# Kernel tuning notes

Hardware: AMD Instinct MI355X
Metric: run time of the kernel (lower is better)

## Reference

```python
import jax, jax.numpy as jnp
import numpy as np

D_MODEL = 1024
NUM_HEADS = 16
HEAD_DIM = D_MODEL // NUM_HEADS


def setup_inputs() -> dict:
    key = jax.random.key(0)
    ks = jax.random.split(key, 9)
    s = 0.02
    return {
        "x": jax.random.normal(ks[0], (4, 2048, D_MODEL), dtype=jnp.float32),
        "Wq": jax.random.normal(ks[1], (D_MODEL, D_MODEL), dtype=jnp.float32) * s,
        "bq": jnp.zeros((D_MODEL,), dtype=jnp.float32),
        "Wk": jax.random.normal(ks[2], (D_MODEL, D_MODEL), dtype=jnp.float32) * s,
        "bk": jnp.zeros((D_MODEL,), dtype=jnp.float32),
        "Wv": jax.random.normal(ks[3], (D_MODEL, D_MODEL), dtype=jnp.float32) * s,
        "bv": jnp.zeros((D_MODEL,), dtype=jnp.float32),
        "Wo": jax.random.normal(ks[4], (D_MODEL, D_MODEL), dtype=jnp.float32) * s,
        "bo": jnp.zeros((D_MODEL,), dtype=jnp.float32),
    }


def reference(x, Wq, bq, Wk, bk, Wv, bv, Wo, bo):
    B, S, D = x.shape
    H, Hd = NUM_HEADS, HEAD_DIM

    def split_heads(t):  # [B,S,D] -> [B,H,S,Hd]
        return t.reshape(B, S, H, Hd).transpose(0, 2, 1, 3)

    q = split_heads(x @ Wq + bq)
    k = split_heads(x @ Wk + bk)
    v = split_heads(x @ Wv + bv)

    scale = 1.0 / jnp.sqrt(jnp.float32(Hd))
    scores = jnp.einsum("bhqd,bhkd->bhqk", q, k) * scale  # [B,H,S,S]
    attn = jax.nn.softmax(scores, axis=-1)
    # dropout(p=0.1) is identity in eval mode
    ctx = jnp.einsum("bhqk,bhkd->bhqd", attn, v)
    ctx = ctx.transpose(0, 2, 1, 3).reshape(B, S, D)
    return ctx @ Wo + bo
```

## Files before the change

### kernel.cpp

```cpp
#include <hip/hip_runtime.h>
#include <hip/hip_bf16.h>

typedef __bf16 bf16;
typedef bf16 bf16x8 __attribute__((ext_vector_type(8)));
typedef bf16 bf16x4v __attribute__((ext_vector_type(4)));
typedef bf16 bf16x2v __attribute__((ext_vector_type(2)));
typedef float f32x4 __attribute__((ext_vector_type(4)));
typedef float f32x16 __attribute__((ext_vector_type(16)));
typedef unsigned int uint;
typedef uint uint4v __attribute__((ext_vector_type(4)));

#define D_MODEL 1024
#define SEQ     2048
#define BATCH   4
#define NHEAD   16
#define HDIM    64
#define MTOK    8192
#define RSZ     ((size_t)MTOK * D_MODEL)
#define QSCALE  0.18033688011112042f

#define GLD16(src, dst)                                                        \
  __builtin_amdgcn_global_load_lds(                                            \
      (const __attribute__((address_space(1))) void*)(src),                    \
      (__attribute__((address_space(3))) void*)(dst), 16, 0, 0)

#define WAITVM(N) asm volatile("s_waitcnt vmcnt(" #N ")" ::: "memory")
#define BAR() __builtin_amdgcn_s_barrier()

#define PSWAP(a, b) asm("v_permlane32_swap_b32 %0, %1" : "+v"(a), "+v"(b))

__device__ __forceinline__ uint pk2(float lo, float hi) {
  bf16x2v h;
  h[0] = (bf16)lo;
  h[1] = (bf16)hi;
  return __builtin_bit_cast(uint, h);
}

__global__ __launch_bounds__(256) void cvt_x_kernel(const float* __restrict__ x,
                                                    bf16* __restrict__ xb) {
  int i = blockIdx.x * 256 + threadIdx.x;
  f32x4 v = ((const f32x4*)x)[i];
  bf16x4v o;
#pragma unroll
  for (int c = 0; c < 4; ++c) o[c] = (bf16)v[c];
  ((bf16x4v*)xb)[i] = o;
}

__global__ __launch_bounds__(256) void wtrans_kernel(
    const float* __restrict__ Wq, const float* __restrict__ Wk,
    const float* __restrict__ Wv, const float* __restrict__ Wo,
    bf16* __restrict__ wt, bf16* __restrict__ wot) {
  __shared__ float t[32][33];
  int z = blockIdx.z;
  const float* W = (z == 0) ? Wq : (z == 1) ? Wk : (z == 2) ? Wv : Wo;
  bf16* dst = (z < 3) ? (wt + (size_t)z * D_MODEL * D_MODEL) : wot;
  int tx = threadIdx.x, ty = threadIdx.y;
  int bx = blockIdx.x * 32, by = blockIdx.y * 32;
#pragma unroll
  for (int j = 0; j < 4; ++j)
    t[ty + j * 8][tx] = W[(size_t)(by + ty + j * 8) * D_MODEL + bx + tx];
  __syncthreads();
#pragma unroll
  for (int j = 0; j < 4; ++j)
    dst[(size_t)(bx + ty + j * 8) * D_MODEL + by + tx] = (bf16)t[tx][ty + j * 8];
}

__global__ __launch_bounds__(256) void vtrans_kernel(const bf16* __restrict__ V,
                                                     bf16* __restrict__ Vt) {
  __shared__ bf16 Ls[128][72];
  const int st = blockIdx.x, bh = blockIdx.y;
  const bf16* src = V + ((size_t)bh * SEQ + st * 128) * HDIM;
  bf16* dst = Vt + (size_t)bh * HDIM * SEQ + st * 128;
  const int t = threadIdx.x;
  const int r = t >> 3, d0 = (t & 7) * 8;
#pragma unroll
  for (int j = 0; j < 4; ++j)
    *(bf16x8*)&Ls[r + j * 32][d0] = *(const bf16x8*)(src + (size_t)(r + j * 32) * HDIM + d0);
  __syncthreads();
  const int d = t & 63, sc = (t >> 6) * 32;
#pragma unroll
  for (int c = 0; c < 4; ++c) {
    bf16x8 v;
#pragma unroll
    for (int i = 0; i < 8; ++i) v[i] = Ls[sc + c * 8 + i][d];
    *(bf16x8*)(dst + (size_t)d * SEQ + sc + c * 8) = v;
  }
}

template <int MODE>
__global__ __launch_bounds__(256) void gemm_bt(
    const bf16* __restrict__ A, const bf16* __restrict__ Bt,
    const float* __restrict__ bias0, const float* __restrict__ bias1,
    const float* __restrict__ bias2, void* __restrict__ outp) {
  __shared__ bf16 As[128 * 32];
  __shared__ bf16 Bs[128 * 32];
  const int tid = threadIdx.x;
  const int wave = tid >> 6, lane = tid & 63;
  const int rowBase = blockIdx.y * 128;
  const int colBase = blockIdx.x * 128;
  const int wR = (wave >> 1) * 64;
  const int wC = (wave & 1) * 64;

  const int r0 = tid >> 2, c0 = tid & 3;
  const int cp0 = c0 ^ ((r0 >> 1) & 3);
  const int r1 = 64 + r0;
  const int cp1 = c0 ^ ((r1 >> 1) & 3);
  const bf16* srcA0 = A + (size_t)(rowBase + r0) * 1024 + cp0 * 8;
  const bf16* srcA1 = A + (size_t)(rowBase + r1) * 1024 + cp1 * 8;
  const bf16* srcB0 = Bt + (size_t)(colBase + r0) * 1024 + cp0 * 8;
  const bf16* srcB1 = Bt + (size_t)(colBase + r1) * 1024 + cp1 * 8;
  char* AsB = (char*)As;
  char* BsB = (char*)Bs;
  char* ldsA0 = AsB + wave * 1024;
  char* ldsA1 = AsB + 4096 + wave * 1024;
  char* ldsB0 = BsB + wave * 1024;
  char* ldsB1 = BsB + 4096 + wave * 1024;

  int aoff[4], boff[4];
#pragma unroll
  for (int i = 0; i < 4; ++i) {
    int ra = wR + i * 16 + (lane & 15);
    aoff[i] = ra * 64 + (((lane >> 4) ^ ((ra >> 1) & 3)) * 16);
    int rb = wC + i * 16 + (lane & 15);
    boff[i] = rb * 64 + (((lane >> 4) ^ ((rb >> 1) & 3)) * 16);
  }

  f32x4 acc[4][4] = {};
  for (int k0 = 0; k0 < 1024; k0 += 32) {
    GLD16(srcA0 + k0, ldsA0);
    GLD16(srcA1 + k0, ldsA1);
    GLD16(srcB0 + k0, ldsB0);
    GLD16(srcB1 + k0, ldsB1);
    __syncthreads();
    bf16x8 af[4], bf_[4];
#pragma unroll
    for (int i = 0; i < 4; ++i) af[i] = *(const bf16x8*)(AsB + aoff[i]);
#pragma unroll
    for (int i = 0; i < 4; ++i) bf_[i] = *(const bf16x8*)(BsB + boff[i]);
#pragma unroll
    for (int mi = 0; mi < 4; ++mi)
#pragma unroll
      for (int ni = 0; ni < 4; ++ni)
        acc[mi][ni] =
            __builtin_amdgcn_mfma_f32_16x16x32_bf16(af[mi], bf_[ni], acc[mi][ni], 0, 0, 0);
    __syncthreads();
  }

  const int rl = (lane >> 4) * 4;
  const int cl = lane & 15;
  if (MODE == 0) {
    bf16* qkvb = (bf16*)outp;
#pragma unroll
    for (int mi = 0; mi < 4; ++mi) {
      int rbase = rowBase + wR + mi * 16 + rl;
#pragma unroll
      for (int ni = 0; ni < 4; ++ni) {
        int col = colBase + wC + ni * 16 + cl;
        int mat = col >> 10, nn = col & 1023;
        int hh = nn >> 6, dd = nn & 63;
        const float* bp = (mat == 0) ? bias0 : (mat == 1) ? bias1 : bias2;
        float scl = (mat == 0) ? QSCALE : 1.0f;
        float bvv = bp[nn];
        bf16* dst = qkvb + (size_t)mat * RSZ;
#pragma unroll
        for (int r = 0; r < 4; ++r) {
          int m = rbase + r;
          int bb = m >> 11, ss = m & 2047;
          dst[((size_t)(bb * NHEAD + hh) * SEQ + ss) * HDIM + dd] =
              (bf16)((acc[mi][ni][r] + bvv) * scl);
        }
      }
    }
  } else {
    float* dst = (float*)outp;
#pragma unroll
    for (int mi = 0; mi < 4; ++mi) {
      int rbase = rowBase + wR + mi * 16 + rl;
#pragma unroll
      for (int ni = 0; ni < 4; ++ni) {
        int col = colBase + wC + ni * 16 + cl;
        float bvv = bias0[col];
#pragma unroll
        for (int r = 0; r < 4; ++r)
          dst[(size_t)(rbase + r) * 1024 + col] = acc[mi][ni][r] + bvv;
      }
    }
  }
}

__global__ __launch_bounds__(256, 3) void attn_kernel(const bf16* __restrict__ qkv,
                                                      const bf16* __restrict__ vt,
                                                      bf16* __restrict__ ctx) {
  __shared__ __align__(16) char smem[32768];
  char* Kbuf = smem;
  char* Vbuf = smem + 16384;

  const int tid = threadIdx.x;
  const int wave = tid >> 6, lane = tid & 63;
  const int l31 = lane & 31, l5 = lane >> 5;
  const int swz = (blockIdx.x & 7) * 128 + (blockIdx.x >> 3);
  const int qt = swz & 15, hh = (swz >> 4) & 15, bb = swz >> 8;
  const int bh = bb * NHEAD + hh;
  const bf16* Qp = qkv + (size_t)bh * SEQ * HDIM;
  const bf16* Kp = qkv + RSZ + (size_t)bh * SEQ * HDIM;
  const bf16* Vtp = vt + (size_t)bh * HDIM * SEQ;

  const int qrow = qt * 128 + wave * 32 + l31;
  bf16x8 qf[4];
#pragma unroll
  for (int kc = 0; kc < 4; ++kc)
    qf[kc] = *(const bf16x8*)(Qp + (size_t)qrow * 64 + kc * 16 + l5 * 8);

  const int sr = tid >> 3;
  const int sz = (tid & 7) ^ (sr & 7);
  const bf16* srcK0 = Kp + sr * 64 + sz * 8;
  const bf16* srcK1 = Kp + (sr + 32) * 64 + sz * 8;
  const bf16* srcV0 = Vtp + (size_t)sr * SEQ + sz * 8;
  const bf16* srcV1 = Vtp + (size_t)(sr + 32) * SEQ + sz * 8;

#define STAGE(sel, t)                                                     \
  do {                                                                    \
    GLD16(srcK0 + (t) * 4096, Kbuf + (sel) * 8192 + wave * 1024);         \
    GLD16(srcK1 + (t) * 4096, Kbuf + (sel) * 8192 + 4096 + wave * 1024);  \
    GLD16(srcV0 + (t) * 64, Vbuf + (sel) * 8192 + wave * 1024);           \
    GLD16(srcV1 + (t) * 64, Vbuf + (sel) * 8192 + 4096 + wave * 1024);    \
  } while (0)

  f32x16 o[2];
#pragma unroll
  for (int nd = 0; nd < 2; ++nd)
#pragma unroll
    for (int r = 0; r < 16; ++r) o[nd][r] = 0.f;
  float m_run = -1e30f, l_run = 0.f;

  STAGE(0, 0);

  for (int kt = 0; kt < 32; ++kt) {
    const int cur = kt & 1;
    if (kt < 31) {
      STAGE(cur ^ 1, kt + 1);
      WAITVM(4);
    } else {
      WAITVM(0);
    }
    BAR();

    const char* Kc = Kbuf + cur * 8192;
    const char* Vc = Vbuf + cur * 8192;

    f32x16 s[2];
#pragma unroll
    for (int nb = 0; nb < 2; ++nb)
#pragma unroll
      for (int r = 0; r < 16; ++r) s[nb][r] = 0.f;
    __builtin_amdgcn_s_setprio(1);
#pragma unroll
    for (int nb = 0; nb < 2; ++nb)
#pragma unroll
      for (int kc = 0; kc < 4; ++kc) {
        int row = nb * 32 + l31;
        int off = row * 128 + (((2 * kc + l5) ^ (row & 7)) * 16);
        bf16x8 kf = *(const bf16x8*)(Kc + off);
        s[nb] = __builtin_amdgcn_mfma_f32_32x32x16_bf16(kf, qf[kc], s[nb], 0, 0, 0);
      }
    __builtin_amdgcn_s_setprio(0);

    float t8[8];
#pragma unroll
    for (int r = 0; r < 8; ++r)
      t8[r] = fmaxf(fmaxf(s[0][r], s[0][r + 8]), fmaxf(s[1][r], s[1][r + 8]));
#pragma unroll
    for (int r = 0; r < 4; ++r) t8[r] = fmaxf(t8[r], t8[r + 4]);
    float pmax = fmaxf(fmaxf(t8[0], t8[1]), fmaxf(t8[2], t8[3]));
    pmax = fmaxf(pmax, __shfl_xor(pmax, 32, 64));

    if (!__all(pmax - m_run <= 8.0f)) {
      float mnew = fmaxf(m_run, pmax);
      float al = __builtin_amdgcn_exp2f(m_run - mnew);
      m_run = mnew;
      l_run *= al;
#pragma unroll
      for (int nd = 0; nd < 2; ++nd)
#pragma unroll
        for (int r = 0; r < 16; ++r) o[nd][r] *= al;
    }
#pragma unroll
    for (int nb = 0; nb < 2; ++nb)
#pragma unroll
      for (int r = 0; r < 16; ++r)
        s[nb][r] = __builtin_amdgcn_exp2f(s[nb][r] - m_run);

    f32x16 tv = s[0] + s[1];
    float q8[8];
#pragma unroll
    for (int r = 0; r < 8; ++r) q8[r] = tv[r] + tv[r + 8];
#pragma unroll
    for (int r = 0; r < 4; ++r) q8[r] += q8[r + 4];
    float rs = (q8[0] + q8[1]) + (q8[2] + q8[3]);
    rs += __shfl_xor(rs, 32, 64);
    l_run += rs;

    bf16x8 pf[4];
#pragma unroll
    for (int cc = 0; cc < 4; ++cc) {
      const int nb = cc >> 1, b0 = (cc & 1) * 8;
      uint w0 = pk2(s[nb][b0 + 0], s[nb][b0 + 1]);
      uint w1 = pk2(s[nb][b0 + 2], s[nb][b0 + 3]);
      uint w2 = pk2(s[nb][b0 + 4], s[nb][b0 + 5]);
      uint w3 = pk2(s[nb][b0 + 6], s[nb][b0 + 7]);
      PSWAP(w0, w2);
      PSWAP(w1, w3);
      uint4v u = {w0, w1, w2, w3};
      pf[cc] = __builtin_bit_cast(bf16x8, u);
    }

    __builtin_amdgcn_s_setprio(1);
#pragma unroll
    for (int nd = 0; nd < 2; ++nd)
#pragma unroll
      for (int cc = 0; cc < 4; ++cc) {
        int row = nd * 32 + l31;
        int off = row * 128 + (((2 * cc + l5) ^ (row & 7)) * 16);
        bf16x8 vf = *(const bf16x8*)(Vc + off);
        o[nd] = __builtin_amdgcn_mfma_f32_32x32x16_bf16(vf, pf[cc], o[nd], 0, 0, 0);
      }
    __builtin_amdgcn_s_setprio(0);
    BAR();
  }

  const float inv = 1.0f / l_run;
  bf16* crow = ctx + (size_t)(bb * SEQ + qrow) * D_MODEL + hh * HDIM;
#pragma unroll
  for (int nd = 0; nd < 2; ++nd)
#pragma unroll
    for (int a = 0; a < 4; ++a) {
      bf16x4v p4;
#pragma unroll
      for (int b = 0; b < 4; ++b) p4[b] = (bf16)(o[nd][4 * a + b] * inv);
      *(bf16x4v*)(crow + nd * 32 + a * 8 + l5 * 4) = p4;
    }
#undef STAGE
}

extern "C" void kernel_launch(void* const* d_in, const int* in_sizes, int n_in,
                              void* d_out, int out_size, void* d_ws, size_t ws_size,
                              hipStream_t stream) {
  const float* x  = (const float*)d_in[0];
  const float* Wq = (const float*)d_in[1];
  const float* bq = (const float*)d_in[2];
  const float* Wk = (const float*)d_in[3];
  const float* bk = (const float*)d_in[4];
  const float* Wv = (const float*)d_in[5];
  const float* bv = (const float*)d_in[6];
  const float* Wo = (const float*)d_in[7];
  const float* bo = (const float*)d_in[8];

  char* ws = (char*)d_ws;
  bf16* xb   = (bf16*)(ws);
  bf16* vtb  = (bf16*)(ws);
  bf16* wt   = (bf16*)(ws + (size_t)16 * 1024 * 1024);
  bf16* wot  = (bf16*)(ws + (size_t)22 * 1024 * 1024);
  bf16* qkvb = (bf16*)(ws + (size_t)24 * 1024 * 1024);
  bf16* ctxb = (bf16*)(ws + (size_t)72 * 1024 * 1024);

  cvt_x_kernel<<<8192, 256, 0, stream>>>(x, xb);
  wtrans_kernel<<<dim3(32, 32, 4), dim3(32, 8), 0, stream>>>(Wq, Wk, Wv, Wo, wt, wot);
  gemm_bt<0><<<dim3(24, 64), 256, 0, stream>>>(xb, wt, bq, bk, bv, (void*)qkvb);
  vtrans_kernel<<<dim3(16, 64), 256, 0, stream>>>(qkvb + 2 * RSZ, vtb);
  attn_kernel<<<1024, 256, 0, stream>>>(qkvb, vtb, ctxb);
  gemm_bt<1><<<dim3(8, 64), 256, 0, stream>>>(ctxb, wot, bo, bo, bo, d_out);
}
```

Baseline: 303.8 us.

## Replace GEMM with 256x256-tile double-buffered 8-wave kernel with quadrant scheduling

Replaces the 128x128, 4-wave, single-buffered GEMM with a 256x256-tile, 512-thread kernel. It double-buffers K=64 slices in 128KB of LDS and splits each tile into four quadrant phases that interleave async global-to-LDS loads with MFMA work, using s_setprio and sched barriers. The larger tile is meant to raise data reuse and hide load latency behind compute. The cost is fewer blocks (384 and 128 on a 256-CU part, which gives wave-quantization imbalance), heavy LDS use, and more register pressure.

```diff
diff --git a/kernel.cpp b/kernel.cpp
--- a/kernel.cpp
+++ b/kernel.cpp
@@ -26,8 +26,11 @@
 
 #define WAITVM(N) asm volatile("s_waitcnt vmcnt(" #N ")" ::: "memory")
 #define BAR() __builtin_amdgcn_s_barrier()
+#define SCHEDBAR() __builtin_amdgcn_sched_barrier(0)
 
 #define PSWAP(a, b) asm("v_permlane32_swap_b32 %0, %1" : "+v"(a), "+v"(b))
+
+#define MFMA16(a, b, c) __builtin_amdgcn_mfma_f32_16x16x32_bf16((a), (b), (c), 0, 0, 0)
 
 __device__ __forceinline__ uint pk2(float lo, float hi) {
   bf16x2v h;
@@ -88,103 +91,183 @@
 }
 
 template <int MODE>
-__global__ __launch_bounds__(256) void gemm_bt(
+__global__ __launch_bounds__(512, 2) void gemm256(
     const bf16* __restrict__ A, const bf16* __restrict__ Bt,
     const float* __restrict__ bias0, const float* __restrict__ bias1,
     const float* __restrict__ bias2, void* __restrict__ outp) {
-  __shared__ bf16 As[128 * 32];
-  __shared__ bf16 Bs[128 * 32];
+  __shared__ __align__(16) char lds[131072];
   const int tid = threadIdx.x;
-  const int wave = tid >> 6, lane = tid & 63;
-  const int rowBase = blockIdx.y * 128;
-  const int colBase = blockIdx.x * 128;
-  const int wR = (wave >> 1) * 64;
-  const int wC = (wave & 1) * 64;
-
-  const int r0 = tid >> 2, c0 = tid & 3;
-  const int cp0 = c0 ^ ((r0 >> 1) & 3);
-  const int r1 = 64 + r0;
-  const int cp1 = c0 ^ ((r1 >> 1) & 3);
-  const bf16* srcA0 = A + (size_t)(rowBase + r0) * 1024 + cp0 * 8;
-  const bf16* srcA1 = A + (size_t)(rowBase + r1) * 1024 + cp1 * 8;
-  const bf16* srcB0 = Bt + (size_t)(colBase + r0) * 1024 + cp0 * 8;
-  const bf16* srcB1 = Bt + (size_t)(colBase + r1) * 1024 + cp1 * 8;
-  char* AsB = (char*)As;
-  char* BsB = (char*)Bs;
-  char* ldsA0 = AsB + wave * 1024;
-  char* ldsA1 = AsB + 4096 + wave * 1024;
-  char* ldsB0 = BsB + wave * 1024;
-  char* ldsB1 = BsB + 4096 + wave * 1024;
-
-  int aoff[4], boff[4];
-#pragma unroll
-  for (int i = 0; i < 4; ++i) {
-    int ra = wR + i * 16 + (lane & 15);
-    aoff[i] = ra * 64 + (((lane >> 4) ^ ((ra >> 1) & 3)) * 16);
-    int rb = wC + i * 16 + (lane & 15);
-    boff[i] = rb * 64 + (((lane >> 4) ^ ((rb >> 1) & 3)) * 16);
+  const int w = tid >> 6, lane = tid & 63;
+  const int l15 = lane & 15, l16 = lane >> 4;
+  const int NX = (MODE == 0) ? 12 : 4;
+  const int bx = blockIdx.x % NX, by = blockIdx.x / NX;
+  const int rowBase = by * 256, colBase = bx * 256;
+
+  const int srow0 = tid >> 3, srow1 = (512 + tid) >> 3;
+  const int sch0 = (tid & 7) ^ (srow0 & 7);
+  const int sch1 = (tid & 7) ^ (srow1 & 7);
+  const bf16* gA = A + (size_t)rowBase * 1024;
+  const bf16* gB = Bt + (size_t)colBase * 1024;
+  const int wb0 = (tid & ~63) * 16;
+  const int wb1 = (512 + (tid & ~63)) * 16;
+
+#define STG_A(b, h, kt)                                                                   \
+  do {                                                                                    \
+    GLD16(gA + (size_t)((h)*128 + srow0) * 1024 + (kt)*64 + sch0 * 8,                     \
+          lds + (b)*32768 + (h)*16384 + wb0);                                             \
+    GLD16(gA + (size_t)((h)*128 + srow1) * 1024 + (kt)*64 + sch1 * 8,                     \
+          lds + (b)*32768 + (h)*16384 + wb1);                                             \
+  } while (0)
+#define STG_B(b, h, kt)                                                                   \
+  do {                                                                                    \
+    GLD16(gB + (size_t)((h)*128 + srow0) * 1024 + (kt)*64 + sch0 * 8,                     \
+          lds + 65536 + (b)*32768 + (h)*16384 + wb0);                                     \
+    GLD16(gB + (size_t)((h)*128 + srow1) * 1024 + (kt)*64 + sch1 * 8,                     \
+          lds + 65536 + (b)*32768 + (h)*16384 + wb1);                                     \
+  } while (0)
+
+  const int arow = (w & 3) * 32 + l15;
+  const int brow = (w >> 2) * 64 + l15;
+  int achk[2];
+#pragma unroll
+  for (int ks = 0; ks < 2; ++ks) achk[ks] = ((ks * 4 + l16) ^ (l15 & 7)) * 16;
+#define AOFF(qm, mi, ks) (((qm)*128 + arow + (mi)*16) * 128 + achk[ks])
+#define BOFF(qn, ni, ks) (((qn)*128 + brow + (ni)*16) * 128 + achk[ks])
+
+  f32x4 acc[2][2][2][4] = {};
+
+  STG_A(0, 0, 0);
+  STG_B(0, 0, 0);
+  STG_A(0, 1, 0);
+  STG_B(0, 1, 0);
+
+#define TILE_BODY(T, SON, W0, W1, W2)                                                     \
+  {                                                                                       \
+    const int cb = (T)&1, nb = cb ^ 1;                                                    \
+    const char* At = lds + cb * 32768;                                                    \
+    const char* Bl = lds + 65536 + cb * 32768;                                            \
+                                          \
+    WAITVM(W0);                                                                           \
+    BAR();                                                                                \
+    if (SON) STG_A(nb, 0, (T) + 1);                                                       \
+    bf16x8 a0f[2][2], b0f[4][2];                                                          \
+    _Pragma("unroll") for (int mi = 0; mi < 2; ++mi)                                      \
+        _Pragma("unroll") for (int ks = 0; ks < 2; ++ks)                                  \
+            a0f[mi][ks] = *(const bf16x8*)(At + AOFF(0, mi, ks));                         \
+    _Pragma("unroll") for (int ni = 0; ni < 4; ++ni)                                      \
+        _Pragma("unroll") for (int ks = 0; ks < 2; ++ks)                                  \
+            b0f[ni][ks] = *(const bf16x8*)(Bl + BOFF(0, ni, ks));                         \
+    __builtin_amdgcn_s_setprio(1);                                                        \
+    _Pragma("unroll") for (int mi = 0; mi < 2; ++mi)                                      \
+        _Pragma("unroll") for (int ni = 0; ni < 4; ++ni) {                                \
+      acc[0][0][mi][ni] = MFMA16(a0f[mi][0], b0f[ni][0], acc[0][0][mi][ni]);              \
+      acc[0][0][mi][ni] = MFMA16(a0f[mi][1], b0f[ni][1], acc[0][0][mi][ni]);              \
+    }                                                                                     \
+    __builtin_amdgcn_s_setprio(0);                                                        \
+    SCHEDBAR();                                                                           \
+                                             \
+    WAITVM(W1);                                                                           \
+    BAR();                                                                                \
+    if (SON) STG_B(nb, 0, (T) + 1);                                                       \
+    bf16x8 a1f[2][2];                                                                     \
+    _Pragma("unroll") for (int mi = 0; mi < 2; ++mi)                                      \
+        _Pragma("unroll") for (int ks = 0; ks < 2; ++ks)                                  \
+            a1f[mi][ks] = *(const bf16x8*)(At + AOFF(1, mi, ks));                         \
+    __builtin_amdgcn_s_setprio(1);                                                        \
+    _Pragma("unroll") for (int mi = 0; mi < 2; ++mi)                                      \
+        _Pragma("unroll") for (int ni = 0; ni < 4; ++ni) {                                \
+      acc[1][0][mi][ni] = MFMA16(a1f[mi][0], b0f[ni][0], acc[1][0][mi][ni]);              \
+      acc[1][0][mi][ni] = MFMA16(a1f[mi][1], b0f[ni][1], acc[1][0][mi][ni]);              \
+    }                                                                                     \
+    __builtin_amdgcn_s_setprio(0);                                                        \
+    SCHEDBAR();                                                                           \
+                                             \
+    WAITVM(W2);                                                                           \
+    BAR();                                                                                \
+    if (SON) STG_A(nb, 1, (T) + 1);                                                       \
+    bf16x8 b1f[4][2];                                                                     \
+    _Pragma("unroll") for (int ni = 0; ni < 4; ++ni)                                      \
+        _Pragma("unroll") for (int ks = 0; ks < 2; ++ks)                                  \
+            b1f[ni][ks] = *(const bf16x8*)(Bl + BOFF(1, ni, ks));                         \
+    __builtin_amdgcn_s_setprio(1);                                                        \
+    _Pragma("unroll") for (int mi = 0; mi < 2; ++mi)                                      \
+        _Pragma("unroll") for (int ni = 0; ni < 4; ++ni) {                                \
+      acc[1][1][mi][ni] = MFMA16(a1f[mi][0], b1f[ni][0], acc[1][1][mi][ni]);              \
+      acc[1][1][mi][ni] = MFMA16(a1f[mi][1], b1f[ni][1], acc[1][1][mi][ni]);              \
+    }                                                                                     \
+    __builtin_amdgcn_s_setprio(0);                                                        \
+    SCHEDBAR();                                                                           \
+                        \
+    if (SON) STG_B(nb, 1, (T) + 1);                                                       \
+    bf16x8 a0g[2][2];                                                                     \
+    _Pragma("unroll") for (int mi = 0; mi < 2; ++mi)                                      \
+        _Pragma("unroll") for (int ks = 0; ks < 2; ++ks)                                  \
+            a0g[mi][ks] = *(const bf16x8*)(At + AOFF(0, mi, ks));                         \
+    __builtin_amdgcn_s_setprio(1);                                                        \
+    _Pragma("unroll") for (int mi = 0; mi < 2; ++mi)                                      \
+        _Pragma("unroll") for (int ni = 0; ni < 4; ++ni) {                                \
+      acc[0][1][mi][ni] = MFMA16(a0g[mi][0], b1f[ni][0], acc[0][1][mi][ni]);              \
+      acc[0][1][mi][ni] = MFMA16(a0g[mi][1], b1f[ni][1], acc[0][1][mi][ni]);              \
+    }                                                                                     \
+    __builtin_amdgcn_s_setprio(0);                                                        \
+    SCHEDBAR();                                                                           \
   }
 
-  f32x4 acc[4][4] = {};
-  for (int k0 = 0; k0 < 1024; k0 += 32) {
-    GLD16(srcA0 + k0, ldsA0);
-    GLD16(srcA1 + k0, ldsA1);
-    GLD16(srcB0 + k0, ldsB0);
-    GLD16(srcB1 + k0, ldsB1);
-    __syncthreads();
-    bf16x8 af[4], bf_[4];
-#pragma unroll
-    for (int i = 0; i < 4; ++i) af[i] = *(const bf16x8*)(AsB + aoff[i]);
-#pragma unroll
-    for (int i = 0; i < 4; ++i) bf_[i] = *(const bf16x8*)(BsB + boff[i]);
-#pragma unroll
-    for (int mi = 0; mi < 4; ++mi)
-#pragma unroll
-      for (int ni = 0; ni < 4; ++ni)
-        acc[mi][ni] =
-            __builtin_amdgcn_mfma_f32_16x16x32_bf16(af[mi], bf_[ni], acc[mi][ni], 0, 0, 0);
-    __syncthreads();
-  }
-
-  const int rl = (lane >> 4) * 4;
-  const int cl = lane & 15;
+  for (int t = 0; t < 15; ++t) TILE_BODY(t, 1, 4, 4, 4);
+  TILE_BODY(15, 0, 4, 2, 0);
+#undef TILE_BODY
+#undef STG_A
+#undef STG_B
+#undef AOFF
+#undef BOFF
+
+  const int rl = l16 * 4;
   if (MODE == 0) {
     bf16* qkvb = (bf16*)outp;
-#pragma unroll
-    for (int mi = 0; mi < 4; ++mi) {
-      int rbase = rowBase + wR + mi * 16 + rl;
-#pragma unroll
-      for (int ni = 0; ni < 4; ++ni) {
-        int col = colBase + wC + ni * 16 + cl;
-        int mat = col >> 10, nn = col & 1023;
-        int hh = nn >> 6, dd = nn & 63;
-        const float* bp = (mat == 0) ? bias0 : (mat == 1) ? bias1 : bias2;
-        float scl = (mat == 0) ? QSCALE : 1.0f;
-        float bvv = bp[nn];
-        bf16* dst = qkvb + (size_t)mat * RSZ;
-#pragma unroll
-        for (int r = 0; r < 4; ++r) {
-          int m = rbase + r;
-          int bb = m >> 11, ss = m & 2047;
-          dst[((size_t)(bb * NHEAD + hh) * SEQ + ss) * HDIM + dd] =
-              (bf16)((acc[mi][ni][r] + bvv) * scl);
-        }
+    const int mat = colBase >> 10;
+    const float* bp = (mat == 0) ? bias0 : (mat == 1) ? bias1 : bias2;
+    const float scl = (mat == 0) ? QSCALE : 1.0f;
+    bf16* dst = qkvb + (size_t)mat * RSZ;
+#pragma unroll
+    for (int qm = 0; qm < 2; ++qm)
+#pragma unroll
+      for (int mi = 0; mi < 2; ++mi) {
+        int rbase = rowBase + qm * 128 + (w & 3) * 32 + mi * 16 + rl;
+#pragma unroll
+        for (int qn = 0; qn < 2; ++qn)
+#pragma unroll
+          for (int ni = 0; ni < 4; ++ni) {
+            int n = colBase + qn * 128 + (w >> 2) * 64 + ni * 16 + l15;
+            int nn = n & 1023;
+            int hh = nn >> 6, dd = nn & 63;
+            float bvv = bp[nn];
+#pragma unroll
+            for (int r = 0; r < 4; ++r) {
+              int m = rbase + r;
+              int bb2 = m >> 11, ss = m & 2047;
+              dst[((size_t)(bb2 * NHEAD + hh) * SEQ + ss) * HDIM + dd] =
+                  (bf16)((acc[qm][qn][mi][ni][r] + bvv) * scl);
+            }
+          }
       }
-    }
   } else {
-    float* dst = (float*)outp;
-#pragma unroll
-    for (int mi = 0; mi < 4; ++mi) {
-      int rbase = rowBase + wR + mi * 16 + rl;
-#pragma unroll
-      for (int ni = 0; ni < 4; ++ni) {
-        int col = colBase + wC + ni * 16 + cl;
-        float bvv = bias0[col];
-#pragma unroll
-        for (int r = 0; r < 4; ++r)
-          dst[(size_t)(rbase + r) * 1024 + col] = acc[mi][ni][r] + bvv;
+    float* dstf = (float*)outp;
+#pragma unroll
+    for (int qm = 0; qm < 2; ++qm)
+#pragma unroll
+      for (int mi = 0; mi < 2; ++mi) {
+        int rbase = rowBase + qm * 128 + (w & 3) * 32 + mi * 16 + rl;
+#pragma unroll
+        for (int qn = 0; qn < 2; ++qn)
+#pragma unroll
+          for (int ni = 0; ni < 4; ++ni) {
+            int n = colBase + qn * 128 + (w >> 2) * 64 + ni * 16 + l15;
+            float bvv = bias0[n];
+#pragma unroll
+            for (int r = 0; r < 4; ++r)
+              dstf[(size_t)(rbase + r) * 1024 + n] = acc[qm][qn][mi][ni][r] + bvv;
+          }
       }
-    }
   }
 }
 
@@ -365,8 +448,8 @@
 
   cvt_x_kernel<<<8192, 256, 0, stream>>>(x, xb);
   wtrans_kernel<<<dim3(32, 32, 4), dim3(32, 8), 0, stream>>>(Wq, Wk, Wv, Wo, wt, wot);
-  gemm_bt<0><<<dim3(24, 64), 256, 0, stream>>>(xb, wt, bq, bk, bv, (void*)qkvb);
+  gemm256<0><<<384, 512, 0, stream>>>(xb, wt, bq, bk, bv, (void*)qkvb);
   vtrans_kernel<<<dim3(16, 64), 256, 0, stream>>>(qkvb + 2 * RSZ, vtb);
   attn_kernel<<<1024, 256, 0, stream>>>(qkvb, vtb, ctxb);
-  gemm_bt<1><<<dim3(8, 64), 256, 0, stream>>>(ctxb, wot, bo, bo, bo, d_out);
-}
+  gemm256<1><<<128, 512, 0, stream>>>(ctxb, wot, bo, bo, bo, d_out);
+}
```

Result: no change. 301.1 us (-0.9%).
